# Performance work log

Measured on AMD Instinct MI355X. Metric: run time of the kernel, lower is better.

## Reference

```python
import jax, jax.numpy as jnp
import numpy as np

H = 8        # num_heads
D = 128      # attention_dim
DV = 128     # linear_dim
B = 8
MAX_SEQLEN = 1024
LENGTHS = np.array([512 + 64 * b for b in range(B)], dtype=np.int64)  # jagged lengths
TOTAL = int(LENGTHS.sum())  # 5888


def setup_inputs() -> dict:
    key = jax.random.key(0)
    k1, k2, k3 = jax.random.split(key, 3)
    offsets = jnp.asarray(np.concatenate([[0], np.cumsum(LENGTHS)]), dtype=jnp.int32)
    tq = jax.random.normal(k1, (TOTAL, H * D), dtype=jnp.float32)
    tk = jax.random.normal(k2, (TOTAL, H * D), dtype=jnp.float32)
    tv = jax.random.normal(k3, (TOTAL, H * DV), dtype=jnp.float32)
    return {"tq": tq, "tk": tk, "tv": tv, "offsets": offsets,
            "max_seqlen": MAX_SEQLEN, "scaling_seqlen": -1}


def reference(tq, tk, tv, offsets, max_seqlen, scaling_seqlen):
    # HSTU jagged causal attention: out = (silu(q k^T * alpha) / n) @ v, per sequence.
    alpha = 1.0 / (D ** 0.5)
    denom = float(scaling_seqlen) if scaling_seqlen > 0 else float(max_seqlen)
    lengths = offsets[1:] - offsets[:-1]            # [B]
    pos = jnp.arange(max_seqlen, dtype=offsets.dtype)
    valid = pos[None, :] < lengths[:, None]          # [B, N] padding mask
    tok = offsets[:-1, None] + pos[None, :]          # [B, N] flat token index
    safe = jnp.where(valid, tok, 0)
    # gather jagged -> padded dense [B, N, H, D]
    q = tq.reshape(-1, H, D)[safe]
    k = tk.reshape(-1, H, D)[safe]
    v = tv.reshape(-1, H, DV)[safe]
    scores = jnp.einsum('bihd,bjhd->bhij', q, k) * alpha   # [B, H, N, N]
    attn = jax.nn.silu(scores) / denom                     # no softmax in HSTU
    causal = pos[:, None] >= pos[None, :]                  # attend to j <= i
    mask = causal[None, None, :, :] & valid[:, None, None, :] & valid[:, None, :, None]
    attn = jnp.where(mask, attn, 0.0)
    out = jnp.einsum('bhij,bjhd->bihd', attn, v)           # [B, N, H, DV]
    out = out * valid[:, :, None, None]
    # scatter padded -> jagged flat (invalid rows contribute zeros to index 0)
    flat = jnp.zeros((tq.shape[0], H, DV), tq.dtype).at[safe.reshape(-1)].add(
        out.reshape(-1, H, DV))
    return flat.reshape(-1, H * DV)
```

## Files before the change

kernel.cpp:

```cpp
#include <hip/hip_runtime.h>
#include <hip/hip_bf16.h>

typedef float f32x4 __attribute__((ext_vector_type(4)));
typedef __bf16 bf16x8 __attribute__((ext_vector_type(8)));
typedef unsigned int u32;
typedef unsigned int u32x2 __attribute__((ext_vector_type(2)));
typedef unsigned short u16;

#define NH 8
#define HD 128
#define ROWE (NH*HD)
#define QB 64
#define JB 32
#define KSTR 148
#define VSTR 36
#define KSZ (JB*KSTR)
#define VSZ (HD*VSTR)

__device__ __forceinline__ u16 bfb(float f) {
  return __builtin_bit_cast(u16, __float2bfloat16(f));
}
__device__ __forceinline__ u32 pk2(float lo, float hi) {
  return (u32)bfb(lo) | ((u32)bfb(hi) << 16);
}

union FR { u32 u[4]; bf16x8 v; };

struct StReg { f32x4 k[4]; f32x4 v[4]; };

__device__ __forceinline__ void unit_cj(int u, int& c, int& j) {
  c = (u & 3) | (((u >> 4) & 7) << 2);
  j = ((u >> 2) & 3) | (((u >> 7) & 7) << 2);
}

__device__ __forceinline__ void stage_load(StReg& s, const float* __restrict__ tk,
    const float* __restrict__ tv, int base_row, int cap, int hoff, int tid) {
#pragma unroll
  for (int it = 0; it < 4; ++it) {
    int c, j; unit_cj(tid + (it << 8), c, j);
    int row = base_row + j; if (row > cap) row = cap;
    size_t g = (size_t)row * ROWE + hoff + 4*c;
    s.k[it] = *(const f32x4*)(tk + g);
    s.v[it] = *(const f32x4*)(tv + g);
  }
}

__device__ __forceinline__ void stage_write(const StReg& s, u16* kw, u16* vw, int tid) {
#pragma unroll
  for (int it = 0; it < 4; ++it) {
    int c, j; unit_cj(tid + (it << 8), c, j);
    u32x2 kp; kp.x = pk2(s.k[it].x, s.k[it].y); kp.y = pk2(s.k[it].z, s.k[it].w);
    *(u32x2*)(&kw[j*KSTR + 4*c]) = kp;
    vw[(4*c+0)*VSTR + j] = bfb(s.v[it].x);
    vw[(4*c+1)*VSTR + j] = bfb(s.v[it].y);
    vw[(4*c+2)*VSTR + j] = bfb(s.v[it].z);
    vw[(4*c+3)*VSTR + j] = bfb(s.v[it].w);
  }
}

__global__ __launch_bounds__(256, 3) void hstu_fwd(
    const float* __restrict__ tq, const float* __restrict__ tk,
    const float* __restrict__ tv, const int* __restrict__ offs,
    const int* __restrict__ pms, const int* __restrict__ pss,
    float* __restrict__ out, int nrows)
{
  __shared__ __align__(16) u16 kbuf[2][KSZ];
  __shared__ __align__(16) u16 vbuf[2][VSZ];

  const int h = blockIdx.x & 7;
  int r = blockIdx.x >> 3;

  int o[9];
#pragma unroll
  for (int i = 0; i < 9; ++i) o[i] = offs[i];

  int selq = -1, soff = 0, sn = 0;
  for (int k = 15; k >= 0; --k) {
#pragma unroll
    for (int b = 0; b < 8; ++b) {
      int nseq = o[b+1] - o[b];
      int ntb = (nseq + 63) >> 6;
      if (k < ntb) {
        if (r == 0 && selq < 0) { selq = k; soff = o[b]; sn = nseq; }
        --r;
      }
    }
  }
  if (selq < 0) return;

  const int cap  = nrows - 1;
  const int q0   = selq * QB;
  const int tid  = threadIdx.x;
  const int lane = tid & 63;
  const int w    = tid >> 6;
  const int lrow = lane & 15;
  const int lgrp = lane >> 4;
  const int hoff = h * HD;

  const float qscale = 0.12751744f;
  int ms = pms[0], ss = pss[0];
  float den = (ss > 0) ? (float)ss : (float)ms;
  const float cs = 0.69314718056f / den;

  FR qf[4];
  {
    int qrow = soff + q0 + 16*w + lrow; if (qrow > cap) qrow = cap;
    const float* qp = tq + (size_t)qrow * ROWE + hoff;
#pragma unroll
    for (int ds = 0; ds < 4; ++ds) {
      f32x4 a = *(const f32x4*)(qp + ds*32 + 4*lgrp);
      f32x4 b = *(const f32x4*)(qp + ds*32 + 4*lgrp + 16);
      qf[ds].u[0] = pk2(a.x*qscale, a.y*qscale);
      qf[ds].u[1] = pk2(a.z*qscale, a.w*qscale);
      qf[ds].u[2] = pk2(b.x*qscale, b.y*qscale);
      qf[ds].u[3] = pk2(b.z*qscale, b.w*qscale);
    }
  }

  f32x4 acc[8];
#pragma unroll
  for (int i = 0; i < 8; ++i) acc[i] = (f32x4){0.f, 0.f, 0.f, 0.f};

  int jend = q0 + QB; if (jend > sn) jend = sn;
  const int ntj = (jend + JB - 1) >> 5;

  StReg st;
  stage_load(st, tk, tv, soff, cap, hoff, tid);
  stage_write(st, kbuf[0], vbuf[0], tid);

  for (int t = 0; t < ntj; ++t) {
    __syncthreads();
    const bool pre = (t + 1 < ntj);
    if (pre) stage_load(st, tk, tv, soff + (t+1)*JB, cap, hoff, tid);

    const int j0 = t * JB;
    if (q0 + 16*w + 15 >= j0) {
      const char* kbc = (const char*)kbuf[t & 1] + lrow*(2*KSTR) + lgrp*8;
      f32x4 s0 = {0,0,0,0}, s1 = {0,0,0,0};
#pragma unroll
      for (int ds = 0; ds < 4; ++ds) {
        FR a0, a1;
        const char* p = kbc + ds*64;
        *(u32x2*)(&a0.u[0]) = *(const u32x2*)(p);
        *(u32x2*)(&a0.u[2]) = *(const u32x2*)(p + 32);
        *(u32x2*)(&a1.u[0]) = *(const u32x2*)(p + 16*2*KSTR);
        *(u32x2*)(&a1.u[2]) = *(const u32x2*)(p + 16*2*KSTR + 32);
        s0 = __builtin_amdgcn_mfma_f32_16x16x32_bf16(a0.v, qf[ds].v, s0, 0, 0, 0);
        s1 = __builtin_amdgcn_mfma_f32_16x16x32_bf16(a1.v, qf[ds].v, s1, 0, 0, 0);
      }

      const int iq  = q0 + 16*w + lrow;
      const int jb0 = j0 + 4*lgrp;
      float pv[8];
#pragma unroll
      for (int rr = 0; rr < 4; ++rr) {
        float y0 = s0[rr], y1 = s1[rr];
        float z0 = __fdividef(y0, 1.f + exp2f(-y0));
        float z1 = __fdividef(y1, 1.f + exp2f(-y1));
        pv[rr]   = (jb0 + rr      <= iq) ? z0 : 0.f;
        pv[rr+4] = (jb0 + 16 + rr <= iq) ? z1 : 0.f;
      }
      FR pf;
      pf.u[0] = pk2(pv[0], pv[1]); pf.u[1] = pk2(pv[2], pv[3]);
      pf.u[2] = pk2(pv[4], pv[5]); pf.u[3] = pk2(pv[6], pv[7]);

      const char* vbc = (const char*)vbuf[t & 1] + lrow*(2*VSTR) + lgrp*8;
#pragma unroll
      for (int sd = 0; sd < 8; ++sd) {
        FR vf;
        const char* p2 = vbc + sd*(16*2*VSTR);
        *(u32x2*)(&vf.u[0]) = *(const u32x2*)(p2);
        *(u32x2*)(&vf.u[2]) = *(const u32x2*)(p2 + 32);
        acc[sd] = __builtin_amdgcn_mfma_f32_16x16x32_bf16(pf.v, vf.v, acc[sd], 0, 0, 0);
      }
    }
    if (pre) stage_write(st, kbuf[(t+1)&1], vbuf[(t+1)&1], tid);
  }

  const int or0 = q0 + 16*w + 4*lgrp;
#pragma unroll
  for (int rr = 0; rr < 4; ++rr) {
    int ir = or0 + rr;
    if (ir < sn) {
      float* op = out + (size_t)(soff + ir) * ROWE + hoff + lrow;
#pragma unroll
      for (int sd = 0; sd < 8; ++sd) op[sd*16] = acc[sd][rr] * cs;
    }
  }
}

extern "C" void kernel_launch(void* const* d_in, const int* in_sizes, int n_in,
                              void* d_out, int out_size, void* d_ws, size_t ws_size,
                              hipStream_t stream) {
  const float* tq = (const float*)d_in[0];
  const float* tk = (const float*)d_in[1];
  const float* tv = (const float*)d_in[2];
  const int* offs = (const int*)d_in[3];
  const int* pms  = (const int*)d_in[4];
  const int* pss  = (const int*)d_in[5];
  float* out = (float*)d_out;

  int nrows = in_sizes[0] / ROWE;
  int nb    = in_sizes[3] - 1;
  int maxtiles = nrows / QB + nb;
  dim3 grid(NH * maxtiles);
  hipLaunchKernelGGL(hstu_fwd, grid, dim3(256), 0, stream,
                     tq, tk, tv, offs, pms, pss, out, nrows);
}
```

Measured before the change: 144.7 us.

## Pre-convert K/V to bf16, split long KV ranges into chunks with atomic accumulation

Adds a prep kernel that converts K and V to bf16 in workspace once and zeroes the output, so the attention kernel stages half the bytes per KV tile. The attention kernel now splits each query tile's KV range into 256-column chunks distributed over a fixed persistent grid, which balances the causal-triangle load across blocks. Tiles needing more than one chunk accumulate into the output with float atomics. The cost is an extra launch plus a full K/V/out memory pass, and atomic traffic for long tiles.

```diff
diff --git a/kernel.cpp b/kernel.cpp
--- a/kernel.cpp
+++ b/kernel.cpp
@@ -5,62 +5,91 @@
 typedef __bf16 bf16x8 __attribute__((ext_vector_type(8)));
 typedef unsigned int u32;
 typedef unsigned int u32x2 __attribute__((ext_vector_type(2)));
+typedef unsigned int u32x4 __attribute__((ext_vector_type(4)));
 typedef unsigned short u16;
 
 #define NH 8
 #define HD 128
-#define ROWE (NH*HD)
+#define ROWE 1024
 #define QB 64
 #define JB 32
+#define JCH 256
+#define RSTRIDE 192
 #define KSTR 148
 #define VSTR 36
 #define KSZ (JB*KSTR)
 #define VSZ (HD*VSTR)
 
-__device__ __forceinline__ u16 bfb(float f) {
+static __device__ __forceinline__ u16 bfb(float f) {
   return __builtin_bit_cast(u16, __float2bfloat16(f));
 }
-__device__ __forceinline__ u32 pk2(float lo, float hi) {
+static __device__ __forceinline__ u32 pk2(float lo, float hi) {
   return (u32)bfb(lo) | ((u32)bfb(hi) << 16);
 }
 
 union FR { u32 u[4]; bf16x8 v; };
 
-struct StReg { f32x4 k[4]; f32x4 v[4]; };
-
-__device__ __forceinline__ void unit_cj(int u, int& c, int& j) {
+__global__ __launch_bounds__(256) void prep_cvt(
+    const float* __restrict__ tk, const float* __restrict__ tv,
+    u16* __restrict__ kb, u16* __restrict__ vb,
+    float* __restrict__ outz, long n8)
+{
+  long idx = (long)blockIdx.x * 256 + threadIdx.x;
+  long stride = (long)gridDim.x * 256;
+  for (long i = idx; i < n8; i += stride) {
+    const f32x4* kp = (const f32x4*)(tk + i * 8);
+    const f32x4* vp = (const f32x4*)(tv + i * 8);
+    f32x4 k0 = kp[0], k1 = kp[1], v0 = vp[0], v1 = vp[1];
+    u32x4 ko, vo;
+    ko.x = pk2(k0.x, k0.y); ko.y = pk2(k0.z, k0.w);
+    ko.z = pk2(k1.x, k1.y); ko.w = pk2(k1.z, k1.w);
+    vo.x = pk2(v0.x, v0.y); vo.y = pk2(v0.z, v0.w);
+    vo.z = pk2(v1.x, v1.y); vo.w = pk2(v1.z, v1.w);
+    *(u32x4*)(kb + i * 8) = ko;
+    *(u32x4*)(vb + i * 8) = vo;
+    f32x4 z = {0.f, 0.f, 0.f, 0.f};
+    ((f32x4*)(outz + i * 8))[0] = z;
+    ((f32x4*)(outz + i * 8))[1] = z;
+  }
+}
+
+static __device__ __forceinline__ void unit_cj(int u, int& c, int& j) {
   c = (u & 3) | (((u >> 4) & 7) << 2);
   j = ((u >> 2) & 3) | (((u >> 7) & 7) << 2);
 }
 
-__device__ __forceinline__ void stage_load(StReg& s, const float* __restrict__ tk,
-    const float* __restrict__ tv, int base_row, int cap, int hoff, int tid) {
+struct StReg { u32x2 k[4]; u32x2 v[4]; };
+
+static __device__ __forceinline__ void stage_load(StReg& s,
+    const u16* __restrict__ kb, const u16* __restrict__ vb,
+    int base_row, int cap, int hoff, int tid) {
 #pragma unroll
   for (int it = 0; it < 4; ++it) {
     int c, j; unit_cj(tid + (it << 8), c, j);
     int row = base_row + j; if (row > cap) row = cap;
-    size_t g = (size_t)row * ROWE + hoff + 4*c;
-    s.k[it] = *(const f32x4*)(tk + g);
-    s.v[it] = *(const f32x4*)(tv + g);
-  }
-}
-
-__device__ __forceinline__ void stage_write(const StReg& s, u16* kw, u16* vw, int tid) {
+    size_t g = (size_t)row * ROWE + hoff + 4 * c;
+    s.k[it] = *(const u32x2*)(kb + g);
+    s.v[it] = *(const u32x2*)(vb + g);
+  }
+}
+
+static __device__ __forceinline__ void stage_write(const StReg& s,
+    u16* kw, u16* vw, int tid) {
 #pragma unroll
   for (int it = 0; it < 4; ++it) {
     int c, j; unit_cj(tid + (it << 8), c, j);
-    u32x2 kp; kp.x = pk2(s.k[it].x, s.k[it].y); kp.y = pk2(s.k[it].z, s.k[it].w);
-    *(u32x2*)(&kw[j*KSTR + 4*c]) = kp;
-    vw[(4*c+0)*VSTR + j] = bfb(s.v[it].x);
-    vw[(4*c+1)*VSTR + j] = bfb(s.v[it].y);
-    vw[(4*c+2)*VSTR + j] = bfb(s.v[it].z);
-    vw[(4*c+3)*VSTR + j] = bfb(s.v[it].w);
+    *(u32x2*)(&kw[j * KSTR + 4 * c]) = s.k[it];
+    u32x2 vv = s.v[it];
+    vw[(4 * c + 0) * VSTR + j] = (u16)(vv.x);
+    vw[(4 * c + 1) * VSTR + j] = (u16)(vv.x >> 16);
+    vw[(4 * c + 2) * VSTR + j] = (u16)(vv.y);
+    vw[(4 * c + 3) * VSTR + j] = (u16)(vv.y >> 16);
   }
 }
 
 __global__ __launch_bounds__(256, 3) void hstu_fwd(
-    const float* __restrict__ tq, const float* __restrict__ tk,
-    const float* __restrict__ tv, const int* __restrict__ offs,
+    const u16* __restrict__ kb, const u16* __restrict__ vb,
+    const float* __restrict__ tq, const int* __restrict__ offs,
     const int* __restrict__ pms, const int* __restrict__ pss,
     float* __restrict__ out, int nrows)
 {
@@ -68,31 +97,17 @@
   __shared__ __align__(16) u16 vbuf[2][VSZ];
 
   const int h = blockIdx.x & 7;
-  int r = blockIdx.x >> 3;
+  const int rblk = blockIdx.x >> 3;
+  const int rstr = gridDim.x >> 3;
 
   int o[9];
 #pragma unroll
   for (int i = 0; i < 9; ++i) o[i] = offs[i];
 
-  int selq = -1, soff = 0, sn = 0;
-  for (int k = 15; k >= 0; --k) {
-#pragma unroll
-    for (int b = 0; b < 8; ++b) {
-      int nseq = o[b+1] - o[b];
-      int ntb = (nseq + 63) >> 6;
-      if (k < ntb) {
-        if (r == 0 && selq < 0) { selq = k; soff = o[b]; sn = nseq; }
-        --r;
-      }
-    }
-  }
-  if (selq < 0) return;
-
-  const int cap  = nrows - 1;
-  const int q0   = selq * QB;
-  const int tid  = threadIdx.x;
+  const int cap = nrows - 1;
+  const int tid = threadIdx.x;
   const int lane = tid & 63;
-  const int w    = tid >> 6;
+  const int w = tid >> 6;
   const int lrow = lane & 15;
   const int lgrp = lane >> 4;
   const int hoff = h * HD;
@@ -102,89 +117,120 @@
   float den = (ss > 0) ? (float)ss : (float)ms;
   const float cs = 0.69314718056f / den;
 
-  FR qf[4];
-  {
-    int qrow = soff + q0 + 16*w + lrow; if (qrow > cap) qrow = cap;
-    const float* qp = tq + (size_t)qrow * ROWE + hoff;
-#pragma unroll
-    for (int ds = 0; ds < 4; ++ds) {
-      f32x4 a = *(const f32x4*)(qp + ds*32 + 4*lgrp);
-      f32x4 b = *(const f32x4*)(qp + ds*32 + 4*lgrp + 16);
-      qf[ds].u[0] = pk2(a.x*qscale, a.y*qscale);
-      qf[ds].u[1] = pk2(a.z*qscale, a.w*qscale);
-      qf[ds].u[2] = pk2(b.x*qscale, b.y*qscale);
-      qf[ds].u[3] = pk2(b.z*qscale, b.w*qscale);
-    }
-  }
-
-  f32x4 acc[8];
-#pragma unroll
-  for (int i = 0; i < 8; ++i) acc[i] = (f32x4){0.f, 0.f, 0.f, 0.f};
-
-  int jend = q0 + QB; if (jend > sn) jend = sn;
-  const int ntj = (jend + JB - 1) >> 5;
-
-  StReg st;
-  stage_load(st, tk, tv, soff, cap, hoff, tid);
-  stage_write(st, kbuf[0], vbuf[0], tid);
-
-  for (int t = 0; t < ntj; ++t) {
+  for (int e = rblk; ; e += rstr) {
+    int r = e, selq = -1, selc = 0, soff = 0, sn = 0;
+    for (int k = 15; k >= 0; --k) {
+      for (int b = 0; b < 8; ++b) {
+        int n = o[b + 1] - o[b];
+        if (k * 64 >= n) continue;
+        int je = k * 64 + 64; if (je > n) je = n;
+        int nc = (je + JCH - 1) >> 8;
+        if (r < nc) { selq = k; selc = r; soff = o[b]; sn = n; k = -1; break; }
+        r -= nc;
+      }
+    }
+    if (selq < 0) break;
+
+    const int q0 = selq * QB;
+    int jend = q0 + QB; if (jend > sn) jend = sn;
+    const int ncq = (jend + JCH - 1) >> 8;
+    const bool direct = (ncq == 1);
+    const int j0c = selc * JCH;
+    int jec = j0c + JCH; if (jec > jend) jec = jend;
+    const int ntt = (jec - j0c + JB - 1) >> 5;
+
+    FR qf[4];
+    {
+      int qr = soff + q0 + 16 * w + lrow; if (qr > cap) qr = cap;
+      const float* qp = tq + (size_t)qr * ROWE + hoff;
+#pragma unroll
+      for (int ds = 0; ds < 4; ++ds) {
+        f32x4 a = *(const f32x4*)(qp + ds * 32 + 4 * lgrp);
+        f32x4 b = *(const f32x4*)(qp + ds * 32 + 4 * lgrp + 16);
+        qf[ds].u[0] = pk2(a.x * qscale, a.y * qscale);
+        qf[ds].u[1] = pk2(a.z * qscale, a.w * qscale);
+        qf[ds].u[2] = pk2(b.x * qscale, b.y * qscale);
+        qf[ds].u[3] = pk2(b.z * qscale, b.w * qscale);
+      }
+    }
+
+    f32x4 acc[8];
+#pragma unroll
+    for (int i = 0; i < 8; ++i) acc[i] = (f32x4){0.f, 0.f, 0.f, 0.f};
+
+    const int iq = q0 + 16 * w + lrow;
+
     __syncthreads();
-    const bool pre = (t + 1 < ntj);
-    if (pre) stage_load(st, tk, tv, soff + (t+1)*JB, cap, hoff, tid);
-
-    const int j0 = t * JB;
-    if (q0 + 16*w + 15 >= j0) {
-      const char* kbc = (const char*)kbuf[t & 1] + lrow*(2*KSTR) + lgrp*8;
-      f32x4 s0 = {0,0,0,0}, s1 = {0,0,0,0};
-#pragma unroll
-      for (int ds = 0; ds < 4; ++ds) {
-        FR a0, a1;
-        const char* p = kbc + ds*64;
-        *(u32x2*)(&a0.u[0]) = *(const u32x2*)(p);
-        *(u32x2*)(&a0.u[2]) = *(const u32x2*)(p + 32);
-        *(u32x2*)(&a1.u[0]) = *(const u32x2*)(p + 16*2*KSTR);
-        *(u32x2*)(&a1.u[2]) = *(const u32x2*)(p + 16*2*KSTR + 32);
-        s0 = __builtin_amdgcn_mfma_f32_16x16x32_bf16(a0.v, qf[ds].v, s0, 0, 0, 0);
-        s1 = __builtin_amdgcn_mfma_f32_16x16x32_bf16(a1.v, qf[ds].v, s1, 0, 0, 0);
-      }
-
-      const int iq  = q0 + 16*w + lrow;
-      const int jb0 = j0 + 4*lgrp;
-      float pv[8];
-#pragma unroll
-      for (int rr = 0; rr < 4; ++rr) {
-        float y0 = s0[rr], y1 = s1[rr];
-        float z0 = __fdividef(y0, 1.f + exp2f(-y0));
-        float z1 = __fdividef(y1, 1.f + exp2f(-y1));
-        pv[rr]   = (jb0 + rr      <= iq) ? z0 : 0.f;
-        pv[rr+4] = (jb0 + 16 + rr <= iq) ? z1 : 0.f;
-      }
-      FR pf;
-      pf.u[0] = pk2(pv[0], pv[1]); pf.u[1] = pk2(pv[2], pv[3]);
-      pf.u[2] = pk2(pv[4], pv[5]); pf.u[3] = pk2(pv[6], pv[7]);
-
-      const char* vbc = (const char*)vbuf[t & 1] + lrow*(2*VSTR) + lgrp*8;
-#pragma unroll
-      for (int sd = 0; sd < 8; ++sd) {
-        FR vf;
-        const char* p2 = vbc + sd*(16*2*VSTR);
-        *(u32x2*)(&vf.u[0]) = *(const u32x2*)(p2);
-        *(u32x2*)(&vf.u[2]) = *(const u32x2*)(p2 + 32);
-        acc[sd] = __builtin_amdgcn_mfma_f32_16x16x32_bf16(pf.v, vf.v, acc[sd], 0, 0, 0);
-      }
-    }
-    if (pre) stage_write(st, kbuf[(t+1)&1], vbuf[(t+1)&1], tid);
-  }
-
-  const int or0 = q0 + 16*w + 4*lgrp;
-#pragma unroll
-  for (int rr = 0; rr < 4; ++rr) {
-    int ir = or0 + rr;
-    if (ir < sn) {
-      float* op = out + (size_t)(soff + ir) * ROWE + hoff + lrow;
-#pragma unroll
-      for (int sd = 0; sd < 8; ++sd) op[sd*16] = acc[sd][rr] * cs;
+    StReg st;
+    stage_load(st, kb, vb, soff + j0c, cap, hoff, tid);
+    stage_write(st, kbuf[0], vbuf[0], tid);
+
+    for (int tt = 0; tt < ntt; ++tt) {
+      __syncthreads();
+      const bool pre = (tt + 1 < ntt);
+      if (pre) stage_load(st, kb, vb, soff + j0c + (tt + 1) * JB, cap, hoff, tid);
+
+      const int j0 = j0c + tt * JB;
+      const int bsel = tt & 1;
+
+      if (iq - lrow + 15 >= j0) {
+        const char* kbc = (const char*)kbuf[bsel] + lrow * (2 * KSTR) + lgrp * 8;
+        f32x4 s0 = {0.f, 0.f, 0.f, 0.f}, s1 = {0.f, 0.f, 0.f, 0.f};
+#pragma unroll
+        for (int ds = 0; ds < 4; ++ds) {
+          FR a0, a1;
+          const char* p = kbc + ds * 64;
+          *(u32x2*)(&a0.u[0]) = *(const u32x2*)(p);
+          *(u32x2*)(&a0.u[2]) = *(const u32x2*)(p + 32);
+          *(u32x2*)(&a1.u[0]) = *(const u32x2*)(p + 16 * 2 * KSTR);
+          *(u32x2*)(&a1.u[2]) = *(const u32x2*)(p + 16 * 2 * KSTR + 32);
+          s0 = __builtin_amdgcn_mfma_f32_16x16x32_bf16(a0.v, qf[ds].v, s0, 0, 0, 0);
+          s1 = __builtin_amdgcn_mfma_f32_16x16x32_bf16(a1.v, qf[ds].v, s1, 0, 0, 0);
+        }
+
+        const int jb0 = j0 + 4 * lgrp;
+        float pv[8];
+#pragma unroll
+        for (int rr = 0; rr < 4; ++rr) {
+          float y0 = s0[rr], y1 = s1[rr];
+          float z0 = __fdividef(y0, 1.f + exp2f(-y0));
+          float z1 = __fdividef(y1, 1.f + exp2f(-y1));
+          pv[rr]     = (jb0 + rr      <= iq) ? z0 : 0.f;
+          pv[rr + 4] = (jb0 + 16 + rr <= iq) ? z1 : 0.f;
+        }
+        FR pf;
+        pf.u[0] = pk2(pv[0], pv[1]); pf.u[1] = pk2(pv[2], pv[3]);
+        pf.u[2] = pk2(pv[4], pv[5]); pf.u[3] = pk2(pv[6], pv[7]);
+
+        const char* vbc = (const char*)vbuf[bsel] + lrow * (2 * VSTR) + lgrp * 8;
+#pragma unroll
+        for (int sd = 0; sd < 8; ++sd) {
+          FR vf;
+          const char* p2 = vbc + sd * (16 * 2 * VSTR);
+          *(u32x2*)(&vf.u[0]) = *(const u32x2*)(p2);
+          *(u32x2*)(&vf.u[2]) = *(const u32x2*)(p2 + 32);
+          acc[sd] = __builtin_amdgcn_mfma_f32_16x16x32_bf16(pf.v, vf.v, acc[sd], 0, 0, 0);
+        }
+      }
+      if (pre) stage_write(st, kbuf[(tt + 1) & 1], vbuf[(tt + 1) & 1], tid);
+    }
+
+    const int or0 = q0 + 16 * w + 4 * lgrp;
+#pragma unroll
+    for (int rr = 0; rr < 4; ++rr) {
+      int ir = or0 + rr;
+      if (ir < sn) {
+        float* op = out + (size_t)(soff + ir) * ROWE + hoff + lrow;
+        if (direct) {
+#pragma unroll
+          for (int sd = 0; sd < 8; ++sd) op[sd * 16] = acc[sd][rr] * cs;
+        } else {
+#pragma unroll
+          for (int sd = 0; sd < 8; ++sd)
+            __hip_atomic_fetch_add(&op[sd * 16], acc[sd][rr] * cs,
+                                   __ATOMIC_RELAXED, __HIP_MEMORY_SCOPE_AGENT);
+        }
+      }
     }
   }
 }
@@ -201,9 +247,12 @@
   float* out = (float*)d_out;
 
   int nrows = in_sizes[0] / ROWE;
-  int nb    = in_sizes[3] - 1;
-  int maxtiles = nrows / QB + nb;
-  dim3 grid(NH * maxtiles);
-  hipLaunchKernelGGL(hstu_fwd, grid, dim3(256), 0, stream,
-                     tq, tk, tv, offs, pms, pss, out, nrows);
-}
+  u16* kbw = (u16*)d_ws;
+  u16* vbw = kbw + (size_t)nrows * ROWE;
+  long n8 = (long)nrows * ROWE / 8;
+
+  hipLaunchKernelGGL(prep_cvt, dim3(2048), dim3(256), 0, stream,
+                     tk, tv, kbw, vbw, out, n8);
+  hipLaunchKernelGGL(hstu_fwd, dim3(NH * RSTRIDE), dim3(256), 0, stream,
+                     kbw, vbw, tq, offs, pms, pss, out, nrows);
+}
```

After: 176.4 us. +21.9%, slower.

## Split KV loop across two warp groups with shared-memory reduction of partial outputs

Applied to the files above, without the earlier changes.

Doubles the block to 512 threads. Two groups of four waves each handle alternating 32-row K/V tiles, and the ring of shared-memory buffers grows from two to four stages. After the loop, group 1 writes its partial accumulators to shared memory and group 0 adds them and stores the output. The aim is to shorten the serial per-block KV loop and raise the number of loads in flight, at the cost of more LDS, an extra reduction pass, and possible pressure on occupancy and registers.

```diff
diff --git a/kernel.cpp b/kernel.cpp
--- a/kernel.cpp
+++ b/kernel.cpp
@@ -34,10 +34,10 @@
 }
 
 __device__ __forceinline__ void stage_load(StReg& s, const float* __restrict__ tk,
-    const float* __restrict__ tv, int base_row, int cap, int hoff, int tid) {
+    const float* __restrict__ tv, int base_row, int cap, int hoff, int tidL) {
 #pragma unroll
   for (int it = 0; it < 4; ++it) {
-    int c, j; unit_cj(tid + (it << 8), c, j);
+    int c, j; unit_cj(tidL + (it << 8), c, j);
     int row = base_row + j; if (row > cap) row = cap;
     size_t g = (size_t)row * ROWE + hoff + 4*c;
     s.k[it] = *(const f32x4*)(tk + g);
@@ -45,10 +45,10 @@
   }
 }
 
-__device__ __forceinline__ void stage_write(const StReg& s, u16* kw, u16* vw, int tid) {
+__device__ __forceinline__ void stage_write(const StReg& s, u16* kw, u16* vw, int tidL) {
 #pragma unroll
   for (int it = 0; it < 4; ++it) {
-    int c, j; unit_cj(tid + (it << 8), c, j);
+    int c, j; unit_cj(tidL + (it << 8), c, j);
     u32x2 kp; kp.x = pk2(s.k[it].x, s.k[it].y); kp.y = pk2(s.k[it].z, s.k[it].w);
     *(u32x2*)(&kw[j*KSTR + 4*c]) = kp;
     vw[(4*c+0)*VSTR + j] = bfb(s.v[it].x);
@@ -58,14 +58,14 @@
   }
 }
 
-__global__ __launch_bounds__(256, 3) void hstu_fwd(
+__global__ __launch_bounds__(512, 4) void hstu_fwd(
     const float* __restrict__ tq, const float* __restrict__ tk,
     const float* __restrict__ tv, const int* __restrict__ offs,
     const int* __restrict__ pms, const int* __restrict__ pss,
     float* __restrict__ out, int nrows)
 {
-  __shared__ __align__(16) u16 kbuf[2][KSZ];
-  __shared__ __align__(16) u16 vbuf[2][VSZ];
+  __shared__ __align__(16) u16 kbuf[4][KSZ];
+  __shared__ __align__(16) u16 vbuf[4][VSZ];
 
   const int h = blockIdx.x & 7;
   int r = blockIdx.x >> 3;
@@ -91,8 +91,11 @@
   const int cap  = nrows - 1;
   const int q0   = selq * QB;
   const int tid  = threadIdx.x;
+  const int tidL = tid & 255;
   const int lane = tid & 63;
   const int w    = tid >> 6;
+  const int s    = w & 3;
+  const int th   = w >> 2;
   const int lrow = lane & 15;
   const int lgrp = lane >> 4;
   const int hoff = h * HD;
@@ -104,7 +107,7 @@
 
   FR qf[4];
   {
-    int qrow = soff + q0 + 16*w + lrow; if (qrow > cap) qrow = cap;
+    int qrow = soff + q0 + 16*s + lrow; if (qrow > cap) qrow = cap;
     const float* qp = tq + (size_t)qrow * ROWE + hoff;
 #pragma unroll
     for (int ds = 0; ds < 4; ++ds) {
@@ -123,68 +126,86 @@
 
   int jend = q0 + QB; if (jend > sn) jend = sn;
   const int ntj = (jend + JB - 1) >> 5;
+  const int iq  = q0 + 16*s + lrow;
+
+  auto compute = [&](int t) {
+    const int j0 = t * JB;
+    if (q0 + 16*s + 15 < j0) return;
+    const int sl = t & 3;
+    const char* kbc = (const char*)kbuf[sl] + lrow*(2*KSTR) + lgrp*8;
+    f32x4 s0 = {0,0,0,0}, s1 = {0,0,0,0};
+#pragma unroll
+    for (int ds = 0; ds < 4; ++ds) {
+      FR a0, a1;
+      const char* p = kbc + ds*64;
+      *(u32x2*)(&a0.u[0]) = *(const u32x2*)(p);
+      *(u32x2*)(&a0.u[2]) = *(const u32x2*)(p + 32);
+      *(u32x2*)(&a1.u[0]) = *(const u32x2*)(p + 16*2*KSTR);
+      *(u32x2*)(&a1.u[2]) = *(const u32x2*)(p + 16*2*KSTR + 32);
+      s0 = __builtin_amdgcn_mfma_f32_16x16x32_bf16(a0.v, qf[ds].v, s0, 0, 0, 0);
+      s1 = __builtin_amdgcn_mfma_f32_16x16x32_bf16(a1.v, qf[ds].v, s1, 0, 0, 0);
+    }
+    const int jb0 = j0 + 4*lgrp;
+    float pv[8];
+#pragma unroll
+    for (int rr = 0; rr < 4; ++rr) {
+      float y0 = s0[rr], y1 = s1[rr];
+      float z0 = __fdividef(y0, 1.f + exp2f(-y0));
+      float z1 = __fdividef(y1, 1.f + exp2f(-y1));
+      pv[rr]   = (jb0 + rr      <= iq) ? z0 : 0.f;
+      pv[rr+4] = (jb0 + 16 + rr <= iq) ? z1 : 0.f;
+    }
+    FR pf;
+    pf.u[0] = pk2(pv[0], pv[1]); pf.u[1] = pk2(pv[2], pv[3]);
+    pf.u[2] = pk2(pv[4], pv[5]); pf.u[3] = pk2(pv[6], pv[7]);
+    const char* vbc = (const char*)vbuf[sl] + lrow*(2*VSTR) + lgrp*8;
+#pragma unroll
+    for (int sd = 0; sd < 8; ++sd) {
+      FR vf;
+      const char* p2 = vbc + sd*(16*2*VSTR);
+      *(u32x2*)(&vf.u[0]) = *(const u32x2*)(p2);
+      *(u32x2*)(&vf.u[2]) = *(const u32x2*)(p2 + 32);
+      acc[sd] = __builtin_amdgcn_mfma_f32_16x16x32_bf16(pf.v, vf.v, acc[sd], 0, 0, 0);
+    }
+  };
 
   StReg st;
-  stage_load(st, tk, tv, soff, cap, hoff, tid);
-  stage_write(st, kbuf[0], vbuf[0], tid);
-
-  for (int t = 0; t < ntj; ++t) {
+  if (th < ntj) {
+    stage_load(st, tk, tv, soff + th*JB, cap, hoff, tidL);
+    stage_write(st, kbuf[th], vbuf[th], tidL);
+  }
+
+  const int U = (ntj + 1) >> 1;
+  for (int u = 0; u < U; ++u) {
     __syncthreads();
-    const bool pre = (t + 1 < ntj);
-    if (pre) stage_load(st, tk, tv, soff + (t+1)*JB, cap, hoff, tid);
-
-    const int j0 = t * JB;
-    if (q0 + 16*w + 15 >= j0) {
-      const char* kbc = (const char*)kbuf[t & 1] + lrow*(2*KSTR) + lgrp*8;
-      f32x4 s0 = {0,0,0,0}, s1 = {0,0,0,0};
-#pragma unroll
-      for (int ds = 0; ds < 4; ++ds) {
-        FR a0, a1;
-        const char* p = kbc + ds*64;
-        *(u32x2*)(&a0.u[0]) = *(const u32x2*)(p);
-        *(u32x2*)(&a0.u[2]) = *(const u32x2*)(p + 32);
-        *(u32x2*)(&a1.u[0]) = *(const u32x2*)(p + 16*2*KSTR);
-        *(u32x2*)(&a1.u[2]) = *(const u32x2*)(p + 16*2*KSTR + 32);
-        s0 = __builtin_amdgcn_mfma_f32_16x16x32_bf16(a0.v, qf[ds].v, s0, 0, 0, 0);
-        s1 = __builtin_amdgcn_mfma_f32_16x16x32_bf16(a1.v, qf[ds].v, s1, 0, 0, 0);
+    const int tl = 2*u + 2 + th;
+    if (tl < ntj) stage_load(st, tk, tv, soff + tl*JB, cap, hoff, tidL);
+    const int tc = 2*u + th;
+    if (tc < ntj) compute(tc);
+    if (tl < ntj) stage_write(st, kbuf[tl & 3], vbuf[tl & 3], tidL);
+  }
+
+  __syncthreads();
+  float* red = (float*)kbuf;
+  if (th == 1) {
+    float* rp = red + ((s * 64 + lane) << 5);
+#pragma unroll
+    for (int i = 0; i < 8; ++i) *(f32x4*)(rp + 4*i) = acc[i];
+  }
+  __syncthreads();
+  if (th == 0) {
+    const float* rp = red + ((s * 64 + lane) << 5);
+#pragma unroll
+    for (int i = 0; i < 8; ++i) acc[i] += *(const f32x4*)(rp + 4*i);
+    const int or0 = q0 + 16*s + 4*lgrp;
+#pragma unroll
+    for (int rr = 0; rr < 4; ++rr) {
+      int ir = or0 + rr;
+      if (ir < sn) {
+        float* op = out + (size_t)(soff + ir) * ROWE + hoff + lrow;
+#pragma unroll
+        for (int sd = 0; sd < 8; ++sd) op[sd*16] = acc[sd][rr] * cs;
       }
-
-      const int iq  = q0 + 16*w + lrow;
-      const int jb0 = j0 + 4*lgrp;
-      float pv[8];
-#pragma unroll
-      for (int rr = 0; rr < 4; ++rr) {
-        float y0 = s0[rr], y1 = s1[rr];
-        float z0 = __fdividef(y0, 1.f + exp2f(-y0));
-        float z1 = __fdividef(y1, 1.f + exp2f(-y1));
-        pv[rr]   = (jb0 + rr      <= iq) ? z0 : 0.f;
-        pv[rr+4] = (jb0 + 16 + rr <= iq) ? z1 : 0.f;
-      }
-      FR pf;
-      pf.u[0] = pk2(pv[0], pv[1]); pf.u[1] = pk2(pv[2], pv[3]);
-      pf.u[2] = pk2(pv[4], pv[5]); pf.u[3] = pk2(pv[6], pv[7]);
-
-      const char* vbc = (const char*)vbuf[t & 1] + lrow*(2*VSTR) + lgrp*8;
-#pragma unroll
-      for (int sd = 0; sd < 8; ++sd) {
-        FR vf;
-        const char* p2 = vbc + sd*(16*2*VSTR);
-        *(u32x2*)(&vf.u[0]) = *(const u32x2*)(p2);
-        *(u32x2*)(&vf.u[2]) = *(const u32x2*)(p2 + 32);
-        acc[sd] = __builtin_amdgcn_mfma_f32_16x16x32_bf16(pf.v, vf.v, acc[sd], 0, 0, 0);
-      }
-    }
-    if (pre) stage_write(st, kbuf[(t+1)&1], vbuf[(t+1)&1], tid);
-  }
-
-  const int or0 = q0 + 16*w + 4*lgrp;
-#pragma unroll
-  for (int rr = 0; rr < 4; ++rr) {
-    int ir = or0 + rr;
-    if (ir < sn) {
-      float* op = out + (size_t)(soff + ir) * ROWE + hoff + lrow;
-#pragma unroll
-      for (int sd = 0; sd < 8; ++sd) op[sd*16] = acc[sd][rr] * cs;
     }
   }
 }
@@ -204,6 +225,6 @@
   int nb    = in_sizes[3] - 1;
   int maxtiles = nrows / QB + nb;
   dim3 grid(NH * maxtiles);
-  hipLaunchKernelGGL(hstu_fwd, grid, dim3(256), 0, stream,
+  hipLaunchKernelGGL(hstu_fwd, grid, dim3(512), 0, stream,
                      tq, tk, tv, offs, pms, pss, out, nrows);
 }
```

New measurement: 145.4 us. No clear change (+0.5%).
